# Kernel optimization log

Measured on AMD Instinct MI355X. Metric: run time of the kernel, lower is better.

Reference implementation:

```python
import jax, jax.numpy as jnp
import numpy as np

N = 50000      # nodes
E = 800000     # edges (before self loops)
D = 128        # input_dim == hidden_dim == out_channels
H = 1          # heads
L = 3          # layers
SLOPE = 0.2    # GATv2 leaky_relu negative slope


def setup_inputs() -> dict:
    key = jax.random.key(0)
    ks = jax.random.split(key, 9)
    x = jax.random.normal(ks[0], (N, D), dtype=jnp.float32)
    edge_index = jax.random.randint(ks[1], (2, E), 0, N, dtype=jnp.int32)
    s = 1.0 / np.sqrt(D).astype(np.float32)
    # stacked per-layer GATv2Conv params (all layers are D -> H*D here)
    Wl = jax.random.normal(ks[2], (L, D, H * D), dtype=jnp.float32) * s   # lin_l weights
    bl = jnp.zeros((L, H * D), dtype=jnp.float32)
    Wr = jax.random.normal(ks[3], (L, D, H * D), dtype=jnp.float32) * s   # lin_r weights
    br = jnp.zeros((L, H * D), dtype=jnp.float32)
    att = jax.random.normal(ks[4], (L, H, D), dtype=jnp.float32) * s      # attention vector
    bias = jnp.zeros((L, H * D), dtype=jnp.float32)                       # conv output bias
    return {"x": x, "edge_index": edge_index, "Wl": Wl, "bl": bl,
            "Wr": Wr, "br": br, "att": att, "bias": bias}


def reference(x, edge_index, Wl, bl, Wr, br, att, bias):
    # add self loops (PyG GATv2Conv default)
    loops = jnp.arange(N, dtype=edge_index.dtype)
    src = jnp.concatenate([edge_index[0], loops])  # [E+N] message sources j
    dst = jnp.concatenate([edge_index[1], loops])  # [E+N] message targets i

    h = x
    for l in range(L):
        xl = (h @ Wl[l] + bl[l]).reshape(N, H, D)   # source transform
        xr = (h @ Wr[l] + br[l]).reshape(N, H, D)   # target transform
        # edge-wise GATv2 score: att . leaky_relu(xl_j + xr_i)
        e = jax.nn.leaky_relu(xl[src] + xr[dst], SLOPE)      # [E+N, H, D]
        score = jnp.einsum('ehd,hd->eh', e, att[l])          # [E+N, H]
        # segment softmax over incoming edges of each dst node
        m = jax.ops.segment_max(score, dst, num_segments=N)  # [N, H]
        p = jnp.exp(score - m[dst])
        denom = jax.ops.segment_sum(p, dst, num_segments=N)
        alpha = p / (denom[dst] + 1e-16)                     # [E+N, H]
        # weighted scatter-aggregate of source features
        msg = xl[src] * alpha[:, :, None]                    # [E+N, H, D]
        h = jax.ops.segment_sum(msg, dst, num_segments=N).reshape(N, H * D) + bias[l]
        h = jax.nn.relu(h)
    return jax.nn.log_softmax(h, axis=1)
```

## Files before the change

### kernel.cpp

```cpp
#include <hip/hip_runtime.h>
#include <cstdint>
#include <cstddef>

#define N_NODES 50000
#define N_EDGES 800000
#define ET (N_EDGES + N_NODES)
#define D 128
#define NLAYERS 3
#define SLOPE 0.2f
#define NB_SCAN ((N_NODES + 1023) / 1024)

typedef __bf16 bf16x8 __attribute__((ext_vector_type(8)));
typedef float  f32x4  __attribute__((ext_vector_type(4)));
typedef float  f32x2  __attribute__((ext_vector_type(2)));

__device__ __forceinline__ unsigned short f2bf_rne(float v) {
    unsigned u = __float_as_uint(v);
    u += 0x7fffu + ((u >> 16) & 1u);
    return (unsigned short)(u >> 16);
}
__device__ __forceinline__ float bf2f(unsigned short h) {
    return __uint_as_float(((unsigned)h) << 16);
}
__device__ __forceinline__ f32x2 unpack_bf2(unsigned u) {
    f32x2 r;
    r.x = __uint_as_float(u << 16);
    r.y = __uint_as_float(u & 0xffff0000u);
    return r;
}

__global__ void prep_kernel(const float* __restrict__ x,
                            const float* __restrict__ Wl,
                            const float* __restrict__ Wr,
                            unsigned short* __restrict__ hhi,
                            unsigned short* __restrict__ hlo,
                            unsigned short* __restrict__ wlh,
                            unsigned short* __restrict__ wll,
                            unsigned short* __restrict__ wrh,
                            int* __restrict__ deg)
{
    int idx = blockIdx.x * blockDim.x + threadIdx.x;
    if (idx < (N_NODES * D) / 4) {
        float4 v = ((const float4*)x)[idx];
        unsigned short h0 = f2bf_rne(v.x), h1 = f2bf_rne(v.y);
        unsigned short h2 = f2bf_rne(v.z), h3 = f2bf_rne(v.w);
        unsigned short l0 = f2bf_rne(v.x - bf2f(h0)), l1 = f2bf_rne(v.y - bf2f(h1));
        unsigned short l2 = f2bf_rne(v.z - bf2f(h2)), l3 = f2bf_rne(v.w - bf2f(h3));
        uint2 hw, lw;
        hw.x = (unsigned)h0 | ((unsigned)h1 << 16);
        hw.y = (unsigned)h2 | ((unsigned)h3 << 16);
        lw.x = (unsigned)l0 | ((unsigned)l1 << 16);
        lw.y = (unsigned)l2 | ((unsigned)l3 << 16);
        ((uint2*)hhi)[idx] = hw;
        ((uint2*)hlo)[idx] = lw;
    }
    if (idx < NLAYERS * D * D) {
        int l   = idx / (D * D);
        int rem = idx - l * D * D;
        int kk  = rem / D;
        int nn  = rem - kk * D;
        int tp  = l * D * D + nn * D + kk;
        float v = Wl[idx];
        unsigned short h = f2bf_rne(v);
        wlh[tp] = h;
        wll[tp] = f2bf_rne(v - bf2f(h));
        wrh[tp] = f2bf_rne(Wr[idx]);
    }
    if (idx < N_NODES) deg[idx] = 0;
}

__global__ void degree_kernel(const int* __restrict__ dstp, int* __restrict__ deg)
{
    int e = blockIdx.x * blockDim.x + threadIdx.x;
    if (e >= ET) return;
    int dt = (e < N_EDGES) ? dstp[e] : e - N_EDGES;
    atomicAdd(deg + dt, 1);
}

__global__ void scan1_kernel(const int* __restrict__ deg,
                             int* __restrict__ incl, int* __restrict__ bsum)
{
    __shared__ int tmp[1024];
    int tid = threadIdx.x;
    int i = blockIdx.x * 1024 + tid;
    int v = (i < N_NODES) ? deg[i] : 0;
    tmp[tid] = v;
    __syncthreads();
    #pragma unroll
    for (int o = 1; o < 1024; o <<= 1) {
        int t = (tid >= o) ? tmp[tid - o] : 0;
        __syncthreads();
        tmp[tid] += t;
        __syncthreads();
    }
    if (i < N_NODES) incl[i] = tmp[tid];
    if (tid == 1023) bsum[blockIdx.x] = tmp[1023];
}

__global__ void scan3_kernel(const int* __restrict__ deg, const int* __restrict__ incl,
                             const int* __restrict__ bsum,
                             int* __restrict__ off, int* __restrict__ cursor)
{
    __shared__ int sb[NB_SCAN + 1];
    int tid = threadIdx.x;
    if (tid < 64) {
        int v = (tid < NB_SCAN) ? bsum[tid] : 0;
        int orig = v;
        #pragma unroll
        for (int o = 1; o < 64; o <<= 1) {
            int t = __shfl_up(v, o, 64);
            if (tid >= o) v += t;
        }
        if (tid < NB_SCAN) sb[tid] = v - orig;
        if (tid == 63)     sb[NB_SCAN] = v;
    }
    __syncthreads();
    int i = blockIdx.x * blockDim.x + tid;
    if (i < N_NODES) {
        int e = incl[i] - deg[i] + sb[i >> 10];
        off[i] = e;
        cursor[i] = e;
    } else if (i == N_NODES) {
        off[N_NODES] = sb[NB_SCAN];
    }
}

__global__ void scatter_kernel(const int* __restrict__ srcp, const int* __restrict__ dstp,
                               int* __restrict__ cursor, int* __restrict__ esrc)
{
    int e = blockIdx.x * blockDim.x + threadIdx.x;
    if (e >= ET) return;
    int s, dt;
    if (e < N_EDGES) { s = srcp[e]; dt = dstp[e]; }
    else             { s = e - N_EDGES; dt = s; }
    int pos = atomicAdd(cursor + dt, 1);
    esrc[pos] = s;
}

#define LOADB(BLH, BLL, BRH, n0)                                          \
    {   size_t boff = (size_t)((n0) + gl) * D + kg * 8;                   \
        _Pragma("unroll")                                                 \
        for (int ks = 0; ks < 4; ks++) {                                  \
            BLH[ks] = *(const bf16x8*)(wlh + boff + ks * 32);             \
            BLL[ks] = *(const bf16x8*)(wll + boff + ks * 32);             \
            BRH[ks] = *(const bf16x8*)(wrh + boff + ks * 32);             \
        } }

#define COMPUTE(BLH, BLL, BRH, t)                                                    \
    {   const int n0 = c0 + (t) * 16;                                                \
        f32x4 accl0 = {0.f,0.f,0.f,0.f}, accr0 = {0.f,0.f,0.f,0.f};                  \
        f32x4 accl1 = {0.f,0.f,0.f,0.f}, accr1 = {0.f,0.f,0.f,0.f};                  \
        _Pragma("unroll")                                                            \
        for (int ks = 0; ks < 4; ks++) {                                             \
            accl0 = __builtin_amdgcn_mfma_f32_16x16x32_bf16(Ah0[ks], BLH[ks], accl0, 0, 0, 0); \
            accl0 = __builtin_amdgcn_mfma_f32_16x16x32_bf16(Al0[ks], BLH[ks], accl0, 0, 0, 0); \
            accl0 = __builtin_amdgcn_mfma_f32_16x16x32_bf16(Ah0[ks], BLL[ks], accl0, 0, 0, 0); \
            accr0 = __builtin_amdgcn_mfma_f32_16x16x32_bf16(Ah0[ks], BRH[ks], accr0, 0, 0, 0); \
            accl1 = __builtin_amdgcn_mfma_f32_16x16x32_bf16(Ah1[ks], BLH[ks], accl1, 0, 0, 0); \
            accl1 = __builtin_amdgcn_mfma_f32_16x16x32_bf16(Al1[ks], BLH[ks], accl1, 0, 0, 0); \
            accl1 = __builtin_amdgcn_mfma_f32_16x16x32_bf16(Ah1[ks], BLL[ks], accl1, 0, 0, 0); \
            accr1 = __builtin_amdgcn_mfma_f32_16x16x32_bf16(Ah1[ks], BRH[ks], accr1, 0, 0, 0); \
        }                                                                            \
        _Pragma("unroll")                                                            \
        for (int r = 0; r < 4; r++) {                                                \
            int row0 = m0 + kg * 4 + r;                                              \
            if (row0 < n) {                                                          \
                xlb[(size_t)row0 * D + n0 + gl] = f2bf_rne(accl0[r] + blc[t]);       \
                xr [(size_t)row0 * D + n0 + gl] = accr0[r] + brc[t];                 \
            }                                                                        \
            int row1 = m0 + 16 + kg * 4 + r;                                         \
            if (row1 < n) {                                                          \
                xlb[(size_t)row1 * D + n0 + gl] = f2bf_rne(accl1[r] + blc[t]);       \
                xr [(size_t)row1 * D + n0 + gl] = accr1[r] + brc[t];                 \
            }                                                                        \
        } }

__global__ __launch_bounds__(256, 2)
void gemm_mfma_kernel(const unsigned short* __restrict__ hhi,
                      const unsigned short* __restrict__ hlo,
                      const unsigned short* __restrict__ wlh,
                      const unsigned short* __restrict__ wll,
                      const unsigned short* __restrict__ wrh,
                      const float* __restrict__ bl, const float* __restrict__ br,
                      unsigned short* __restrict__ xlb, float* __restrict__ xr, int n)
{
    int lane = threadIdx.x & 63;
    int wid  = threadIdx.x >> 6;
    int rowB = blockIdx.x >> 1;
    int c0   = (blockIdx.x & 1) * 64;
    int m0   = (rowB * 4 + wid) * 32;
    if (m0 >= n) return;
    int gl = lane & 15;
    int kg = lane >> 4;

    float blc[4], brc[4];
    #pragma unroll
    for (int t = 0; t < 4; t++) {
        blc[t] = bl[c0 + t * 16 + gl];
        brc[t] = br[c0 + t * 16 + gl];
    }

    int ar0 = m0 + gl;      if (ar0 >= n) ar0 = n - 1;
    int ar1 = m0 + 16 + gl; if (ar1 >= n) ar1 = n - 1;
    const unsigned short* ah0 = hhi + (size_t)ar0 * D + kg * 8;
    const unsigned short* al0 = hlo + (size_t)ar0 * D + kg * 8;
    const unsigned short* ah1 = hhi + (size_t)ar1 * D + kg * 8;
    const unsigned short* al1 = hlo + (size_t)ar1 * D + kg * 8;
    bf16x8 Ah0[4], Al0[4], Ah1[4], Al1[4];
    #pragma unroll
    for (int ks = 0; ks < 4; ks++) {
        Ah0[ks] = *(const bf16x8*)(ah0 + ks * 32);
        Al0[ks] = *(const bf16x8*)(al0 + ks * 32);
        Ah1[ks] = *(const bf16x8*)(ah1 + ks * 32);
        Al1[ks] = *(const bf16x8*)(al1 + ks * 32);
    }

    bf16x8 B0lh[4], B0ll[4], B0rh[4];
    bf16x8 B1lh[4], B1ll[4], B1rh[4];

    LOADB(B0lh, B0ll, B0rh, c0);
    LOADB(B1lh, B1ll, B1rh, c0 + 16);
    COMPUTE(B0lh, B0ll, B0rh, 0);
    LOADB(B0lh, B0ll, B0rh, c0 + 32);
    COMPUTE(B1lh, B1ll, B1rh, 1);
    LOADB(B1lh, B1ll, B1rh, c0 + 48);
    COMPUTE(B0lh, B0ll, B0rh, 2);
    COMPUTE(B1lh, B1ll, B1rh, 3);
}

template <int LAST>
__global__ void node_attn_kernel(const unsigned short* __restrict__ xlb,
                                 const float* __restrict__ xr,
                                 const float* __restrict__ att,
                                 const float* __restrict__ bias,
                                 const int* __restrict__ off,
                                 const int* __restrict__ esrc,
                                 float* __restrict__ outF,
                                 unsigned short* __restrict__ hhi,
                                 unsigned short* __restrict__ hlo)
{
    int i    = (int)((blockIdx.x * (size_t)blockDim.x + threadIdx.x) >> 6);
    int lane = threadIdx.x & 63;
    if (i >= N_NODES) return;
    int g  = lane >> 4;
    int gl = lane & 15;
    int fb = gl * 8;

    f32x2 aa[4], rr[4];
    {
        float4 a0 = *(const float4*)(att + fb);
        float4 a1 = *(const float4*)(att + fb + 4);
        const float* xri = xr + (size_t)i * D + fb;
        float4 r0 = *(const float4*)(xri);
        float4 r1 = *(const float4*)(xri + 4);
        aa[0] = (f32x2){a0.x, a0.y}; aa[1] = (f32x2){a0.z, a0.w};
        aa[2] = (f32x2){a1.x, a1.y}; aa[3] = (f32x2){a1.z, a1.w};
        rr[0] = (f32x2){r0.x, r0.y}; rr[1] = (f32x2){r0.z, r0.w};
        rr[2] = (f32x2){r1.x, r1.y}; rr[3] = (f32x2){r1.z, r1.w};
    }

    float m = -1e30f, l = 0.f;
    f32x2 acc[4];
    #pragma unroll
    for (int j = 0; j < 4; j++) acc[j] = (f32x2){0.f, 0.f};

    int k    = off[i];
    int kEnd = off[i + 1];

    int kk = k + g;
    bool valid = kk < kEnd;
    int s0 = esrc[valid ? kk : kEnd - 1];
    uint4 x4 = *(const uint4*)(xlb + (size_t)s0 * D + fb);

    while (k < kEnd) {
        int kn = k + 4;
        uint4 nx4 = x4;
        bool nvalid = false;
        if (kn < kEnd) {
            int nkk = kn + g;
            nvalid = nkk < kEnd;
            int ns = esrc[nvalid ? nkk : kEnd - 1];
            nx4 = *(const uint4*)(xlb + (size_t)ns * D + fb);
        }
        f32x2 xx[4];
        xx[0] = unpack_bf2(x4.x); xx[1] = unpack_bf2(x4.y);
        xx[2] = unpack_bf2(x4.z); xx[3] = unpack_bf2(x4.w);
        f32x2 sc2 = {0.f, 0.f};
        #pragma unroll
        for (int j = 0; j < 4; j++) {
            f32x2 v  = xx[j] + rr[j];
            f32x2 lv = __builtin_elementwise_max(v, v * SLOPE);
            sc2 = sc2 + lv * aa[j];
        }
        float sc = sc2.x + sc2.y;
        sc += __shfl_xor(sc, 1, 64);
        sc += __shfl_xor(sc, 2, 64);
        sc += __shfl_xor(sc, 4, 64);
        sc += __shfl_xor(sc, 8, 64);
        if (__any(sc > m + 8.f)) {
            float mn = fmaxf(m, sc);
            float f  = __expf(m - mn);
            float p  = valid ? __expf(sc - mn) : 0.f;
            l = l * f + p;
            f32x2 fv = {f, f}, pv = {p, p};
            #pragma unroll
            for (int j = 0; j < 4; j++) acc[j] = acc[j] * fv + xx[j] * pv;
            m = mn;
        } else {
            float p = valid ? __expf(sc - m) : 0.f;
            l += p;
            f32x2 pv = {p, p};
            #pragma unroll
            for (int j = 0; j < 4; j++) acc[j] = acc[j] + xx[j] * pv;
        }
        x4 = nx4; valid = nvalid;
        k = kn;
    }

    #pragma unroll
    for (int o = 16; o <= 32; o <<= 1) {
        float mo  = __shfl_xor(m, o, 64);
        float lo2 = __shfl_xor(l, o, 64);
        float mn  = fmaxf(m, mo);
        float f1  = __expf(m - mn);
        float f2s = __expf(mo - mn);
        l = l * f1 + lo2 * f2s;
        f32x2 f1v = {f1, f1}, f2v = {f2s, f2s};
        #pragma unroll
        for (int j = 0; j < 4; j++) {
            f32x2 ao;
            ao.x = __shfl_xor(acc[j].x, o, 64);
            ao.y = __shfl_xor(acc[j].y, o, 64);
            acc[j] = acc[j] * f1v + ao * f2v;
        }
        m = mn;
    }

    float inv = 1.f / (l + 1e-16f);
    f32x2 hv[4];
    {
        float4 b0 = *(const float4*)(bias + fb);
        float4 b1 = *(const float4*)(bias + fb + 4);
        f32x2 iv = {inv, inv}, z = {0.f, 0.f};
        f32x2 bb0 = {b0.x, b0.y}, bb1 = {b0.z, b0.w};
        f32x2 bb2 = {b1.x, b1.y}, bb3 = {b1.z, b1.w};
        hv[0] = __builtin_elementwise_max(acc[0] * iv + bb0, z);
        hv[1] = __builtin_elementwise_max(acc[1] * iv + bb1, z);
        hv[2] = __builtin_elementwise_max(acc[2] * iv + bb2, z);
        hv[3] = __builtin_elementwise_max(acc[3] * iv + bb3, z);
    }

    if (LAST) {
        float mx = fmaxf(hv[0].x, hv[0].y);
        #pragma unroll
        for (int j = 1; j < 4; j++) mx = fmaxf(mx, fmaxf(hv[j].x, hv[j].y));
        mx = fmaxf(mx, __shfl_xor(mx, 1, 64));
        mx = fmaxf(mx, __shfl_xor(mx, 2, 64));
        mx = fmaxf(mx, __shfl_xor(mx, 4, 64));
        mx = fmaxf(mx, __shfl_xor(mx, 8, 64));
        float se = 0.f;
        #pragma unroll
        for (int j = 0; j < 4; j++) se += __expf(hv[j].x - mx) + __expf(hv[j].y - mx);
        se += __shfl_xor(se, 1, 64);
        se += __shfl_xor(se, 2, 64);
        se += __shfl_xor(se, 4, 64);
        se += __shfl_xor(se, 8, 64);
        float ls = logf(se) + mx;
        if (g == 0) {
            float4 o0 = make_float4(hv[0].x - ls, hv[0].y - ls, hv[1].x - ls, hv[1].y - ls);
            float4 o1 = make_float4(hv[2].x - ls, hv[2].y - ls, hv[3].x - ls, hv[3].y - ls);
            float* dst = outF + (size_t)i * D + fb;
            *(float4*)(dst)     = o0;
            *(float4*)(dst + 4) = o1;
        }
    } else {
        if (g < 2) {
            unsigned pk[4];
            #pragma unroll
            for (int j = 0; j < 4; j++) {
                float v0 = hv[j].x, v1 = hv[j].y;
                unsigned short h0 = f2bf_rne(v0), h1 = f2bf_rne(v1);
                if (g == 0) pk[j] = (unsigned)h0 | ((unsigned)h1 << 16);
                else {
                    unsigned short l0 = f2bf_rne(v0 - bf2f(h0));
                    unsigned short l1 = f2bf_rne(v1 - bf2f(h1));
                    pk[j] = (unsigned)l0 | ((unsigned)l1 << 16);
                }
            }
            unsigned short* dst = (g == 0 ? hhi : hlo) + (size_t)i * D + fb;
            *(uint4*)dst = make_uint4(pk[0], pk[1], pk[2], pk[3]);
        }
    }
}

extern "C" void kernel_launch(void* const* d_in, const int* in_sizes, int n_in,
                              void* d_out, int out_size, void* d_ws, size_t ws_size,
                              hipStream_t stream)
{
    const float* x    = (const float*)d_in[0];
    const int*   ei   = (const int*)  d_in[1];
    const float* Wl   = (const float*)d_in[2];
    const float* bl   = (const float*)d_in[3];
    const float* Wr   = (const float*)d_in[4];
    const float* br   = (const float*)d_in[5];
    const float* att  = (const float*)d_in[6];
    const float* bias = (const float*)d_in[7];
    float* out = (float*)d_out;

    const int* srcp = ei;
    const int* dstp = ei + N_EDGES;

    const size_t ND = (size_t)N_NODES * D;
    const size_t WSZ = (size_t)NLAYERS * D * D;
    char* ws = (char*)d_ws;
    unsigned short* xlb = (unsigned short*)ws; ws += ND * sizeof(unsigned short);
    float* xr  = (float*)ws;                   ws += ND * sizeof(float);
    unsigned short* hhi = (unsigned short*)ws; ws += ND * sizeof(unsigned short);
    unsigned short* hlo = (unsigned short*)ws; ws += ND * sizeof(unsigned short);
    unsigned short* wlh = (unsigned short*)ws; ws += WSZ * sizeof(unsigned short);
    unsigned short* wll = (unsigned short*)ws; ws += WSZ * sizeof(unsigned short);
    unsigned short* wrh = (unsigned short*)ws; ws += WSZ * sizeof(unsigned short);
    int* deg    = (int*)ws;  ws += (size_t)N_NODES * sizeof(int);
    int* incl   = (int*)ws;  ws += (size_t)N_NODES * sizeof(int);
    int* off    = (int*)ws;  ws += (size_t)(N_NODES + 1) * sizeof(int);
    int* cursor = (int*)ws;  ws += (size_t)N_NODES * sizeof(int);
    int* bsum   = (int*)ws;  ws += (size_t)NB_SCAN * sizeof(int);
    int* esrc   = (int*)ws;  ws += (size_t)ET * sizeof(int);

    const int prepGrid  = (int)((ND / 4 + 255) / 256);
    const int edgeGrid  = (ET + 255) / 256;
    const int gemmGrid  = ((N_NODES + 127) / 128) * 2;
    const int nodeGrid  = (N_NODES + 3) / 4;
    const int scan3Grid = (N_NODES + 1 + 255) / 256;

    prep_kernel<<<prepGrid, 256, 0, stream>>>(x, Wl, Wr, hhi, hlo, wlh, wll, wrh, deg);

    degree_kernel<<<edgeGrid, 256, 0, stream>>>(dstp, deg);
    scan1_kernel<<<NB_SCAN, 1024, 0, stream>>>(deg, incl, bsum);
    scan3_kernel<<<scan3Grid, 256, 0, stream>>>(deg, incl, bsum, off, cursor);
    scatter_kernel<<<edgeGrid, 256, 0, stream>>>(srcp, dstp, cursor, esrc);

    for (int l = 0; l < NLAYERS; l++) {
        size_t wOff = (size_t)l * D * D;
        gemm_mfma_kernel<<<gemmGrid, 256, 0, stream>>>(
            hhi, hlo, wlh + wOff, wll + wOff, wrh + wOff,
            bl + (size_t)l * D, br + (size_t)l * D, xlb, xr, N_NODES);

        if (l == NLAYERS - 1) {
            node_attn_kernel<1><<<nodeGrid, 256, 0, stream>>>(
                xlb, xr, att + (size_t)l * D, bias + (size_t)l * D,
                off, esrc, out, nullptr, nullptr);
        } else {
            node_attn_kernel<0><<<nodeGrid, 256, 0, stream>>>(
                xlb, xr, att + (size_t)l * D, bias + (size_t)l * D,
                off, esrc, nullptr, hhi, hlo);
        }
    }
}
```

Before: 375.2 us.

## Store xr in bf16, restructure GEMM loop order, fuse degree count into prep

The xr target transform is now stored as bf16 instead of fp32, which halves its write traffic in the GEMM and its read traffic in the attention kernel, at some cost in precision of the score. The GEMM is reorganised to iterate over k-slices outermost, keeping all 16 accumulators live and loading B fragments inline instead of double-buffering them through macros. The degree-counting atomics are folded into prep_kernel, and deg is zeroed with hipMemsetAsync, which removes one launch. The larger accumulator set may raise register pressure under the two-block launch bound.

```diff
diff --git a/kernel.cpp b/kernel.cpp
--- a/kernel.cpp
+++ b/kernel.cpp
@@ -32,6 +32,7 @@
 __global__ void prep_kernel(const float* __restrict__ x,
                             const float* __restrict__ Wl,
                             const float* __restrict__ Wr,
+                            const int* __restrict__ dstp,
                             unsigned short* __restrict__ hhi,
                             unsigned short* __restrict__ hlo,
                             unsigned short* __restrict__ wlh,
@@ -66,15 +67,10 @@
         wll[tp] = f2bf_rne(v - bf2f(h));
         wrh[tp] = f2bf_rne(Wr[idx]);
     }
-    if (idx < N_NODES) deg[idx] = 0;
-}
-
-__global__ void degree_kernel(const int* __restrict__ dstp, int* __restrict__ deg)
-{
-    int e = blockIdx.x * blockDim.x + threadIdx.x;
-    if (e >= ET) return;
-    int dt = (e < N_EDGES) ? dstp[e] : e - N_EDGES;
-    atomicAdd(deg + dt, 1);
+    if (idx < ET) {
+        int dt = (idx < N_EDGES) ? dstp[idx] : idx - N_EDGES;
+        atomicAdd(deg + dt, 1);
+    }
 }
 
 __global__ void scan1_kernel(const int* __restrict__ deg,
@@ -137,44 +133,6 @@
     esrc[pos] = s;
 }
 
-#define LOADB(BLH, BLL, BRH, n0)                                          \
-    {   size_t boff = (size_t)((n0) + gl) * D + kg * 8;                   \
-        _Pragma("unroll")                                                 \
-        for (int ks = 0; ks < 4; ks++) {                                  \
-            BLH[ks] = *(const bf16x8*)(wlh + boff + ks * 32);             \
-            BLL[ks] = *(const bf16x8*)(wll + boff + ks * 32);             \
-            BRH[ks] = *(const bf16x8*)(wrh + boff + ks * 32);             \
-        } }
-
-#define COMPUTE(BLH, BLL, BRH, t)                                                    \
-    {   const int n0 = c0 + (t) * 16;                                                \
-        f32x4 accl0 = {0.f,0.f,0.f,0.f}, accr0 = {0.f,0.f,0.f,0.f};                  \
-        f32x4 accl1 = {0.f,0.f,0.f,0.f}, accr1 = {0.f,0.f,0.f,0.f};                  \
-        _Pragma("unroll")                                                            \
-        for (int ks = 0; ks < 4; ks++) {                                             \
-            accl0 = __builtin_amdgcn_mfma_f32_16x16x32_bf16(Ah0[ks], BLH[ks], accl0, 0, 0, 0); \
-            accl0 = __builtin_amdgcn_mfma_f32_16x16x32_bf16(Al0[ks], BLH[ks], accl0, 0, 0, 0); \
-            accl0 = __builtin_amdgcn_mfma_f32_16x16x32_bf16(Ah0[ks], BLL[ks], accl0, 0, 0, 0); \
-            accr0 = __builtin_amdgcn_mfma_f32_16x16x32_bf16(Ah0[ks], BRH[ks], accr0, 0, 0, 0); \
-            accl1 = __builtin_amdgcn_mfma_f32_16x16x32_bf16(Ah1[ks], BLH[ks], accl1, 0, 0, 0); \
-            accl1 = __builtin_amdgcn_mfma_f32_16x16x32_bf16(Al1[ks], BLH[ks], accl1, 0, 0, 0); \
-            accl1 = __builtin_amdgcn_mfma_f32_16x16x32_bf16(Ah1[ks], BLL[ks], accl1, 0, 0, 0); \
-            accr1 = __builtin_amdgcn_mfma_f32_16x16x32_bf16(Ah1[ks], BRH[ks], accr1, 0, 0, 0); \
-        }                                                                            \
-        _Pragma("unroll")                                                            \
-        for (int r = 0; r < 4; r++) {                                                \
-            int row0 = m0 + kg * 4 + r;                                              \
-            if (row0 < n) {                                                          \
-                xlb[(size_t)row0 * D + n0 + gl] = f2bf_rne(accl0[r] + blc[t]);       \
-                xr [(size_t)row0 * D + n0 + gl] = accr0[r] + brc[t];                 \
-            }                                                                        \
-            int row1 = m0 + 16 + kg * 4 + r;                                         \
-            if (row1 < n) {                                                          \
-                xlb[(size_t)row1 * D + n0 + gl] = f2bf_rne(accl1[r] + blc[t]);       \
-                xr [(size_t)row1 * D + n0 + gl] = accr1[r] + brc[t];                 \
-            }                                                                        \
-        } }
-
 __global__ __launch_bounds__(256, 2)
 void gemm_mfma_kernel(const unsigned short* __restrict__ hhi,
                       const unsigned short* __restrict__ hlo,
@@ -182,7 +140,8 @@
                       const unsigned short* __restrict__ wll,
                       const unsigned short* __restrict__ wrh,
                       const float* __restrict__ bl, const float* __restrict__ br,
-                      unsigned short* __restrict__ xlb, float* __restrict__ xr, int n)
+                      unsigned short* __restrict__ xlb, unsigned short* __restrict__ xrb,
+                      int n)
 {
     int lane = threadIdx.x & 63;
     int wid  = threadIdx.x >> 6;
@@ -206,31 +165,59 @@
     const unsigned short* al0 = hlo + (size_t)ar0 * D + kg * 8;
     const unsigned short* ah1 = hhi + (size_t)ar1 * D + kg * 8;
     const unsigned short* al1 = hlo + (size_t)ar1 * D + kg * 8;
-    bf16x8 Ah0[4], Al0[4], Ah1[4], Al1[4];
+
+    f32x4 accl[2][4], accr[2][4];
+    #pragma unroll
+    for (int rt = 0; rt < 2; rt++)
+        #pragma unroll
+        for (int t = 0; t < 4; t++) {
+            accl[rt][t] = (f32x4){0.f, 0.f, 0.f, 0.f};
+            accr[rt][t] = (f32x4){0.f, 0.f, 0.f, 0.f};
+        }
+
     #pragma unroll
     for (int ks = 0; ks < 4; ks++) {
-        Ah0[ks] = *(const bf16x8*)(ah0 + ks * 32);
-        Al0[ks] = *(const bf16x8*)(al0 + ks * 32);
-        Ah1[ks] = *(const bf16x8*)(ah1 + ks * 32);
-        Al1[ks] = *(const bf16x8*)(al1 + ks * 32);
-    }
-
-    bf16x8 B0lh[4], B0ll[4], B0rh[4];
-    bf16x8 B1lh[4], B1ll[4], B1rh[4];
-
-    LOADB(B0lh, B0ll, B0rh, c0);
-    LOADB(B1lh, B1ll, B1rh, c0 + 16);
-    COMPUTE(B0lh, B0ll, B0rh, 0);
-    LOADB(B0lh, B0ll, B0rh, c0 + 32);
-    COMPUTE(B1lh, B1ll, B1rh, 1);
-    LOADB(B1lh, B1ll, B1rh, c0 + 48);
-    COMPUTE(B0lh, B0ll, B0rh, 2);
-    COMPUTE(B1lh, B1ll, B1rh, 3);
+        bf16x8 aH0 = *(const bf16x8*)(ah0 + ks * 32);
+        bf16x8 aL0 = *(const bf16x8*)(al0 + ks * 32);
+        bf16x8 aH1 = *(const bf16x8*)(ah1 + ks * 32);
+        bf16x8 aL1 = *(const bf16x8*)(al1 + ks * 32);
+        #pragma unroll
+        for (int t = 0; t < 4; t++) {
+            size_t boff = (size_t)(c0 + t * 16 + gl) * D + kg * 8 + ks * 32;
+            bf16x8 bLH = *(const bf16x8*)(wlh + boff);
+            bf16x8 bLL = *(const bf16x8*)(wll + boff);
+            bf16x8 bRH = *(const bf16x8*)(wrh + boff);
+            accl[0][t] = __builtin_amdgcn_mfma_f32_16x16x32_bf16(aH0, bLH, accl[0][t], 0, 0, 0);
+            accl[0][t] = __builtin_amdgcn_mfma_f32_16x16x32_bf16(aL0, bLH, accl[0][t], 0, 0, 0);
+            accl[0][t] = __builtin_amdgcn_mfma_f32_16x16x32_bf16(aH0, bLL, accl[0][t], 0, 0, 0);
+            accr[0][t] = __builtin_amdgcn_mfma_f32_16x16x32_bf16(aH0, bRH, accr[0][t], 0, 0, 0);
+            accl[1][t] = __builtin_amdgcn_mfma_f32_16x16x32_bf16(aH1, bLH, accl[1][t], 0, 0, 0);
+            accl[1][t] = __builtin_amdgcn_mfma_f32_16x16x32_bf16(aL1, bLH, accl[1][t], 0, 0, 0);
+            accl[1][t] = __builtin_amdgcn_mfma_f32_16x16x32_bf16(aH1, bLL, accl[1][t], 0, 0, 0);
+            accr[1][t] = __builtin_amdgcn_mfma_f32_16x16x32_bf16(aH1, bRH, accr[1][t], 0, 0, 0);
+        }
+    }
+
+    #pragma unroll
+    for (int rt = 0; rt < 2; rt++) {
+        #pragma unroll
+        for (int t = 0; t < 4; t++) {
+            int col = c0 + t * 16 + gl;
+            #pragma unroll
+            for (int r = 0; r < 4; r++) {
+                int row = m0 + rt * 16 + kg * 4 + r;
+                if (row < n) {
+                    xlb[(size_t)row * D + col] = f2bf_rne(accl[rt][t][r] + blc[t]);
+                    xrb[(size_t)row * D + col] = f2bf_rne(accr[rt][t][r] + brc[t]);
+                }
+            }
+        }
+    }
 }
 
 template <int LAST>
 __global__ void node_attn_kernel(const unsigned short* __restrict__ xlb,
-                                 const float* __restrict__ xr,
+                                 const unsigned short* __restrict__ xrb,
                                  const float* __restrict__ att,
                                  const float* __restrict__ bias,
                                  const int* __restrict__ off,
@@ -250,13 +237,11 @@
     {
         float4 a0 = *(const float4*)(att + fb);
         float4 a1 = *(const float4*)(att + fb + 4);
-        const float* xri = xr + (size_t)i * D + fb;
-        float4 r0 = *(const float4*)(xri);
-        float4 r1 = *(const float4*)(xri + 4);
         aa[0] = (f32x2){a0.x, a0.y}; aa[1] = (f32x2){a0.z, a0.w};
         aa[2] = (f32x2){a1.x, a1.y}; aa[3] = (f32x2){a1.z, a1.w};
-        rr[0] = (f32x2){r0.x, r0.y}; rr[1] = (f32x2){r0.z, r0.w};
-        rr[2] = (f32x2){r1.x, r1.y}; rr[3] = (f32x2){r1.z, r1.w};
+        uint4 r4 = *(const uint4*)(xrb + (size_t)i * D + fb);
+        rr[0] = unpack_bf2(r4.x); rr[1] = unpack_bf2(r4.y);
+        rr[2] = unpack_bf2(r4.z); rr[3] = unpack_bf2(r4.w);
     }
 
     float m = -1e30f, l = 0.f;
@@ -414,7 +399,7 @@
     const size_t WSZ = (size_t)NLAYERS * D * D;
     char* ws = (char*)d_ws;
     unsigned short* xlb = (unsigned short*)ws; ws += ND * sizeof(unsigned short);
-    float* xr  = (float*)ws;                   ws += ND * sizeof(float);
+    unsigned short* xrb = (unsigned short*)ws; ws += ND * sizeof(unsigned short);
     unsigned short* hhi = (unsigned short*)ws; ws += ND * sizeof(unsigned short);
     unsigned short* hlo = (unsigned short*)ws; ws += ND * sizeof(unsigned short);
     unsigned short* wlh = (unsigned short*)ws; ws += WSZ * sizeof(unsigned short);
@@ -433,9 +418,10 @@
     const int nodeGrid  = (N_NODES + 3) / 4;
     const int scan3Grid = (N_NODES + 1 + 255) / 256;
 
-    prep_kernel<<<prepGrid, 256, 0, stream>>>(x, Wl, Wr, hhi, hlo, wlh, wll, wrh, deg);
-
-    degree_kernel<<<edgeGrid, 256, 0, stream>>>(dstp, deg);
+    hipMemsetAsync(deg, 0, (size_t)N_NODES * sizeof(int), stream);
+    prep_kernel<<<prepGrid, 256, 0, stream>>>(x, Wl, Wr, dstp,
+                                              hhi, hlo, wlh, wll, wrh, deg);
+
     scan1_kernel<<<NB_SCAN, 1024, 0, stream>>>(deg, incl, bsum);
     scan3_kernel<<<scan3Grid, 256, 0, stream>>>(deg, incl, bsum, off, cursor);
     scatter_kernel<<<edgeGrid, 256, 0, stream>>>(srcp, dstp, cursor, esrc);
@@ -444,15 +430,15 @@
         size_t wOff = (size_t)l * D * D;
         gemm_mfma_kernel<<<gemmGrid, 256, 0, stream>>>(
             hhi, hlo, wlh + wOff, wll + wOff, wrh + wOff,
-            bl + (size_t)l * D, br + (size_t)l * D, xlb, xr, N_NODES);
+            bl + (size_t)l * D, br + (size_t)l * D, xlb, xrb, N_NODES);
 
         if (l == NLAYERS - 1) {
             node_attn_kernel<1><<<nodeGrid, 256, 0, stream>>>(
-                xlb, xr, att + (size_t)l * D, bias + (size_t)l * D,
+                xlb, xrb, att + (size_t)l * D, bias + (size_t)l * D,
                 off, esrc, out, nullptr, nullptr);
         } else {
             node_attn_kernel<0><<<nodeGrid, 256, 0, stream>>>(
-                xlb, xr, att + (size_t)l * D, bias + (size_t)l * D,
+                xlb, xrb, att + (size_t)l * D, bias + (size_t)l * D,
                 off, esrc, nullptr, hhi, hlo);
         }
     }
```

Result: no change. 377.6 us (+0.6%).
